# Kernel optimization log

Hardware: AMD Instinct MI355X
Metric: run time of the kernel (lower is better)

Reference implementation:

```python
import jax, jax.numpy as jnp
import numpy as np

B, S, D = 8, 4096, 1024
H = 16
HD = D // H          # 64
FF = 128             # FeedForward default intermediate_size
EPS = 1e-6           # flax RMSNorm default


def _rmsnorm(x, g):
    return x * jax.lax.rsqrt(jnp.mean(x * x, axis=-1, keepdims=True) + EPS) * g


def setup_inputs() -> dict:
    key = jax.random.key(0)
    ks = jax.random.split(key, 12)
    s = 0.02
    return {
        "x": jax.random.normal(ks[0], (B, S, D), jnp.float32),
        "attention_mask": jnp.ones((B, HD), jnp.int32),
        # per-head QKV projections stacked over heads: [H, D, HD]
        "Wq": jax.random.normal(ks[1], (H, D, HD), jnp.float32) * s,
        "bq": jnp.zeros((H, HD), jnp.float32),
        "Wk": jax.random.normal(ks[2], (H, D, HD), jnp.float32) * s,
        "bk": jnp.zeros((H, HD), jnp.float32),
        "Wv": jax.random.normal(ks[3], (H, D, HD), jnp.float32) * s,
        "bv": jnp.zeros((H, HD), jnp.float32),
        "Wo": jax.random.normal(ks[4], (D, D), jnp.float32) * s,
        "bo": jnp.zeros((D,), jnp.float32),
        "W1": jax.random.normal(ks[5], (D, FF), jnp.float32) * s,
        "b1": jnp.zeros((FF,), jnp.float32),
        "W2": jax.random.normal(ks[6], (FF, D), jnp.float32) * s,
        "b2": jnp.zeros((D,), jnp.float32),
        "g1": jnp.ones((D,), jnp.float32),
        "g2": jnp.ones((D,), jnp.float32),
    }


def reference(x, attention_mask, Wq, bq, Wk, bk, Wv, bv, Wo, bo, W1, b1, W2, b2, g1, g2):
    # per-head projections, vectorized over heads: [B, H, S, HD]
    q = jnp.einsum('bsd,hde->bhse', x, Wq) + bq[:, None, :]
    k = jnp.einsum('bsd,hde->bhse', x, Wk) + bk[:, None, :]
    v = jnp.einsum('bsd,hde->bhse', x, Wv) + bv[:, None, :]
    # scores = k^T @ q -> [B, H, HD(kfeat), HD(qfeat)]  (feature-feature attention)
    scores = jnp.einsum('bhsk,bhsq->bhkq', k, q)
    # tiled mask: each row of [HD, HD] equals mask -> masks along last (q-feature) axis
    m = attention_mask[:, None, None, :]  # [B,1,1,HD]
    scores = jnp.where(m == 0, -jnp.inf, scores)
    w = jax.nn.softmax(scores / jnp.sqrt(jnp.float32(HD)), axis=-2)
    # out = v @ w -> [B, H, S, HD]
    attn = jnp.einsum('bhsk,bhkq->bhsq', v, w)
    attn = attn.transpose(0, 2, 1, 3).reshape(B, S, D)  # concat heads
    # output projection + residual + RMSNorm
    h = x + attn @ Wo + bo
    h = _rmsnorm(h, g1)
    # tanh FFN + residual + RMSNorm
    ff = jnp.tanh(h @ W1 + b1) @ W2 + b2
    out = _rmsnorm(h + ff, g2)
    return out
```

## Files before the change

### kernel.cpp

```cpp
#include <hip/hip_runtime.h>
#include <math.h>

typedef __attribute__((ext_vector_type(4))) float f32x4;
typedef __attribute__((ext_vector_type(8))) short short8;
typedef __attribute__((ext_vector_type(4))) short short4v;

__device__ __forceinline__ float b2f(unsigned short u) {
  unsigned int x = ((unsigned int)u) << 16;
  return __builtin_bit_cast(float, x);
}
__device__ __forceinline__ unsigned short f2b(float f) {
  unsigned int x = __builtin_bit_cast(unsigned int, f);
  x += 0x7fffu + ((x >> 16) & 1u);
  return (unsigned short)(x >> 16);
}

__device__ __forceinline__ void gload16(const unsigned short* g, unsigned short* l) {
  __builtin_amdgcn_global_load_lds(
      (__attribute__((address_space(1))) void*)(unsigned long long)(const void*)g,
      (__attribute__((address_space(3))) void*)l, 16, 0, 0);
}

#define BARR  { __builtin_amdgcn_sched_barrier(0); __builtin_amdgcn_s_barrier(); __builtin_amdgcn_sched_barrier(0); }
#define LBARR { __builtin_amdgcn_sched_barrier(0); asm volatile("s_waitcnt lgkmcnt(0)" ::: "memory"); __builtin_amdgcn_s_barrier(); __builtin_amdgcn_sched_barrier(0); }
#define VMW(n) { __builtin_amdgcn_sched_barrier(0); asm volatile("s_waitcnt vmcnt(" #n ")" ::: "memory"); __builtin_amdgcn_sched_barrier(0); }

__global__ __launch_bounds__(256) void prep_kernel(
    const float* __restrict__ x, unsigned short* __restrict__ xb,
    const float* __restrict__ Wq, const float* __restrict__ Wk,
    const float* __restrict__ Wv, const float* __restrict__ Wo,
    const float* __restrict__ W1, const float* __restrict__ W2,
    const float* __restrict__ bq, const float* __restrict__ bk, const float* __restrict__ bv,
    const float* __restrict__ g1,
    unsigned short* __restrict__ BqkT, unsigned short* __restrict__ WoT,
    unsigned short* __restrict__ W1T, unsigned short* __restrict__ W2T,
    unsigned short* __restrict__ WvR,
    float* __restrict__ bqkv) {
  __shared__ float tile[64][65];
  int nb = blockIdx.x, t = threadIdx.x;
  if (nb < 16384) {
    long i = (long)nb * 256 + t;
    f32x4 a = ((const f32x4*)x)[i * 2];
    f32x4 b = ((const f32x4*)x)[i * 2 + 1];
    short8 o;
#pragma unroll
    for (int j = 0; j < 4; ++j) { o[j] = (short)f2b(a[j]); o[4 + j] = (short)f2b(b[j]); }
    ((short8*)xb)[i] = o;
    return;
  }
  int n0 = nb - 16384;
  if (n0 == 1088) {
#pragma unroll
    for (int it = 0; it < 12; ++it) {
      int idx = it * 256 + t;
      float v = (idx < 1024) ? bq[idx] : (idx < 2048 ? bk[idx - 1024] : bv[idx - 2048]);
      bqkv[idx] = v;
    }
    return;
  }
  if (n0 >= 832) {
    int rem = n0 - 832, h = rem >> 4, dc = rem & 15;
    int r = t >> 2, c0 = (t & 3) * 16;
    const float* s = Wv + ((long)h * 1024 + dc * 64 + r) * 64 + c0;
    unsigned short* d = WvR + (long)(dc * 64 + r) * 1024 + h * 64 + c0;
#pragma unroll
    for (int j4 = 0; j4 < 4; ++j4) {
      f32x4 v = *(const f32x4*)(s + j4 * 4);
      short4v o;
#pragma unroll
      for (int j = 0; j < 4; ++j) o[j] = (short)f2b(v[j]);
      *(short4v*)(d + j4 * 4) = o;
    }
    return;
  }
  const float* src; unsigned short* dst; int sld, dld;
  bool foldg = false; int dbase = 0;
  if (n0 < 512) {
    int w = n0 >> 8, rem = n0 & 255, h = rem >> 4, dc = rem & 15;
    const float* W = (w == 0) ? Wq : Wk;
    src = W + ((long)h * 1024 + dc * 64) * 64;                 sld = 64;
    dst = BqkT + (long)(w * 1024 + h * 64) * 1024 + dc * 64;   dld = 1024;
  } else if (n0 < 768) {
    int rem = n0 - 512, dr = rem >> 4, jc = rem & 15;
    src = Wo + (long)dr * 64 * 1024 + jc * 64;                 sld = 1024;
    dst = WoT + (long)jc * 64 * 1024 + dr * 64;                dld = 1024;
  } else if (n0 < 800) {
    int rem = n0 - 768, dr = rem >> 1, fc = rem & 1;
    src = W1 + (long)dr * 64 * 128 + fc * 64;                  sld = 128;
    dst = W1T + (long)fc * 64 * 1024 + dr * 64;                dld = 1024;
    foldg = true; dbase = dr * 64;
  } else {
    int rem = n0 - 800, fr = rem >> 4, jc = rem & 15;
    src = W2 + (long)fr * 64 * 1024 + jc * 64;                 sld = 1024;
    dst = W2T + (long)jc * 64 * 128 + fr * 64;                 dld = 128;
  }
  int r = t >> 2, c0 = (t & 3) * 16;
#pragma unroll
  for (int j4 = 0; j4 < 4; ++j4) {
    f32x4 v = *(const f32x4*)(src + (long)r * sld + c0 + j4 * 4);
    tile[c0 + j4 * 4 + 0][r] = v[0];
    tile[c0 + j4 * 4 + 1][r] = v[1];
    tile[c0 + j4 * 4 + 2][r] = v[2];
    tile[c0 + j4 * 4 + 3][r] = v[3];
  }
  __syncthreads();
  short8 o0, o1;
#pragma unroll
  for (int j = 0; j < 8; ++j) {
    float v0 = tile[r][c0 + j], v1 = tile[r][c0 + 8 + j];
    if (foldg) { v0 *= g1[dbase + c0 + j]; v1 *= g1[dbase + c0 + 8 + j]; }
    o0[j] = (short)f2b(v0);
    o1[j] = (short)f2b(v1);
  }
  *(short8*)(dst + (long)r * dld + c0) = o0;
  *(short8*)(dst + (long)r * dld + c0 + 8) = o1;
}

__device__ __forceinline__ void rdA2(short8 (&dst)[4][2], const char* paK0,
                                     const char* paK1, int off) {
#pragma unroll
  for (int fr = 0; fr < 4; ++fr) {
    dst[fr][0] = *(const short8*)(paK0 + off + fr * 2048);
    dst[fr][1] = *(const short8*)(paK1 + off + fr * 2048);
  }
}
__device__ __forceinline__ void rdB2(short8 (&dst)[2][2], const char* pbK0,
                                     const char* pbK1, int off) {
#pragma unroll
  for (int gr = 0; gr < 2; ++gr) {
    dst[gr][0] = *(const short8*)(pbK0 + off + gr * 2048);
    dst[gr][1] = *(const short8*)(pbK1 + off + gr * 2048);
  }
}
template <int BPH>
__device__ __forceinline__ void mfmaq_f(const short8 (&afr)[4][2], const short8 (&bf)[2][2],
                                        f32x4 (*ac)[4]) {
  __builtin_amdgcn_s_setprio(1);
#pragma unroll
  for (int fi = 0; fi < 4; ++fi)
#pragma unroll
    for (int gj = 0; gj < 2; ++gj)
#pragma unroll
      for (int ks = 0; ks < 2; ++ks)
        ac[fi][BPH * 2 + gj] = __builtin_amdgcn_mfma_f32_16x16x32_bf16(
            afr[fi][ks], bf[gj][ks], ac[fi][BPH * 2 + gj], 0, 0, 0);
  __builtin_amdgcn_s_setprio(0);
}

template <int EPI, int BSEL, int BBIAS>
__global__ __launch_bounds__(512, 2) void gemm8p(
    const unsigned short* __restrict__ A, int lda,
    const unsigned short* __restrict__ Bt, int ldb,
    unsigned short* __restrict__ C, int ldc,
    const float* __restrict__ bias,
    const unsigned short* __restrict__ residb, int ldr,
    const float* __restrict__ rs, const float* __restrict__ g1f,
    int K, int NBX) {
  extern __shared__ char smb[];
  const int tid = threadIdx.x;
  const int lane = tid & 63, wid = tid >> 6;
  const int wm = wid >> 2, wn = wid & 3;

  int orig = blockIdx.x;
  int xcd = orig & 7, j = orig >> 3;
  int perx = gridDim.x >> 3;
  int mpx = perx / NBX;
  int ms = j / (4 * NBX), nb = (j >> 2) % NBX, mq = j & 3;
  const long m0 = (long)(xcd * mpx + ms * 4 + mq) * 256;
  const long n0 = (long)nb * 256;
  const unsigned short* bt = BSEL ? (Bt + (m0 >> 12) * 1048576) : Bt;
  const float* biasp = BBIAS ? (bias + (m0 >> 12) * 1024) : bias;

  const int NT = K >> 6, NI = NT >> 1;

  const int lr = lane & 15, lc = (lane >> 4) * 16;
  const int eA = lc ^ ((lr & 7) << 4);
  const char* paK0 = smb + wm * 8192 + lr * 128 + eA;
  const char* paK1 = smb + wm * 8192 + lr * 128 + (eA ^ 64);
  const char* pbK0 = smb + 65536 + wn * 4096 + lr * 128 + eA;
  const char* pbK1 = smb + 65536 + wn * 4096 + lr * 128 + (eA ^ 64);

  short8 afr0[4][2], afr1[4][2];
  short8 bfr0[2][2], bfr1[2][2];
  f32x4 acc[8][4] = {};

  auto stA = [&](int buf, int ph, int kt) {
#pragma unroll
    for (int rnd = 0; rnd < 2; ++rnd) {
      int o = rnd * 8192 + tid * 16;
      int wms = o >> 13, rsw = (o >> 7) & 63, cb = o & 127;
      int pcb = cb ^ ((rsw & 7) << 4);
      const unsigned short* src = A + (m0 + wms * 128 + ph * 64 + rsw) * (long)lda + kt * 64 + (pcb >> 1);
      gload16(src, (unsigned short*)(smb + buf * 32768 + ph * 16384 + o));
    }
  };
  auto stB = [&](int buf, int ph, int kt) {
#pragma unroll
    for (int rnd = 0; rnd < 2; ++rnd) {
      int o = rnd * 8192 + tid * 16;
      int wns = (o >> 12) & 3, rsw = (o >> 7) & 31, cb = o & 127;
      int pcb = cb ^ ((rsw & 7) << 4);
      const unsigned short* src = bt + (n0 + wns * 64 + ph * 32 + rsw) * (long)ldb + kt * 64 + (pcb >> 1);
      gload16(src, (unsigned short*)(smb + 65536 + buf * 32768 + ph * 16384 + o));
    }
  };

  stA(0, 0, 0); stA(0, 1, 0); stB(0, 0, 0); stB(0, 1, 0);
  stA(1, 0, 1); stA(1, 1, 1); stB(1, 0, 1); stB(1, 1, 1);
  VMW(8);
  BARR;
  rdA2(afr0, paK0, paK1, 0);
  rdB2(bfr0, pbK0, pbK1, 0);

  for (int i = 0; i < NI; ++i) {
    int t2 = 2 * i + 2, t3 = 2 * i + 3;
    bool more = t2 < NT;
    LBARR;
    rdB2(bfr1, pbK0, pbK1, 16384);
    mfmaq_f<0>(afr0, bfr0, &acc[0]);
    LBARR;
    rdA2(afr1, paK0, paK1, 16384);
    mfmaq_f<1>(afr0, bfr1, &acc[0]);
    LBARR;
    if (more) { stA(0, 0, t2); stA(0, 1, t2); }
    mfmaq_f<0>(afr1, bfr0, &acc[4]);
    if (more) { VMW(4); } else { VMW(0); }
    LBARR;
    rdA2(afr0, paK0, paK1, 32768);
    rdB2(bfr0, pbK0, pbK1, 32768);
    if (more) { stB(0, 0, t2); stB(0, 1, t2); }
    mfmaq_f<1>(afr1, bfr1, &acc[4]);
    LBARR;
    rdB2(bfr1, pbK0, pbK1, 32768 + 16384);
    mfmaq_f<0>(afr0, bfr0, &acc[0]);
    LBARR;
    rdA2(afr1, paK0, paK1, 32768 + 16384);
    mfmaq_f<1>(afr0, bfr1, &acc[0]);
    LBARR;
    if (more) { stA(1, 0, t3); stA(1, 1, t3); }
    mfmaq_f<0>(afr1, bfr0, &acc[4]);
    if (more) { VMW(4); } else { VMW(0); }
    LBARR;
    if (more) { rdA2(afr0, paK0, paK1, 0); rdB2(bfr0, pbK0, pbK1, 0); }
    if (more) { stB(1, 0, t3); stB(1, 1, t3); }
    mfmaq_f<1>(afr1, bfr1, &acc[4]);
  }

#pragma unroll
  for (int f = 0; f < 8; ++f) {
#pragma unroll
    for (int g = 0; g < 4; ++g) {
      long col = n0 + wn * 64 + g * 16 + (lane & 15);
      float bv = (EPI == 6) ? 0.0f : biasp[col];
      float gv = (EPI == 5) ? g1f[col] : 0.0f;
#pragma unroll
      for (int r = 0; r < 4; ++r) {
        long row = m0 + wm * 128 + f * 16 + (lane >> 4) * 4 + r;
        float o = acc[f][g][r] + bv;
        if (EPI == 3) o += b2f(residb[row * (long)ldr + col]);
        if (EPI == 5) o += b2f(residb[row * (long)ldr + col]) * rs[row] * gv;
        C[row * (long)ldc + col] = f2b(o);
      }
    }
  }
}

template <int EPI>
__global__ __launch_bounds__(256, 2) void gemm_bt(
    const unsigned short* __restrict__ A, int lda,
    const unsigned short* __restrict__ Bt, int ldb,
    unsigned short* __restrict__ C, int ldc,
    const float* __restrict__ bias, const float* __restrict__ rs, int K) {
  __shared__ __align__(16) unsigned short Asm[128 * 32];
  __shared__ __align__(16) unsigned short Bsm[128 * 32];
  const int tid = threadIdx.x;
  const int lane = tid & 63, wid = tid >> 6;
  const int wr = wid >> 1, wc = wid & 1;
  const long m0 = (long)blockIdx.y * 128;
  const long n0 = (long)blockIdx.x * 128;

  f32x4 acc[4][4] = {};

  for (int kk = 0; kk < K; kk += 32) {
    __syncthreads();
#pragma unroll
    for (int i = 0; i < 2; ++i) {
      int slot = i * 256 + tid;
      int r = slot >> 2, cg = (slot & 3) * 8;
      gload16(A + (m0 + r) * (long)lda + kk + cg, &Asm[slot * 8]);
      gload16(Bt + (n0 + r) * (long)ldb + kk + cg, &Bsm[slot * 8]);
    }
    __syncthreads();
    short8 af[4], bfr[4];
#pragma unroll
    for (int mt = 0; mt < 4; ++mt)
      af[mt] = *(const short8*)&Asm[(wr * 64 + mt * 16 + (lane & 15)) * 32 + (lane >> 4) * 8];
#pragma unroll
    for (int nt = 0; nt < 4; ++nt)
      bfr[nt] = *(const short8*)&Bsm[(wc * 64 + nt * 16 + (lane & 15)) * 32 + (lane >> 4) * 8];
#pragma unroll
    for (int mt = 0; mt < 4; ++mt)
#pragma unroll
      for (int nt = 0; nt < 4; ++nt)
        acc[mt][nt] = __builtin_amdgcn_mfma_f32_16x16x32_bf16(af[mt], bfr[nt], acc[mt][nt], 0, 0, 0);
  }

  const long row0 = m0 + wr * 64 + ((lane >> 4) * 4);
  const long col0 = n0 + wc * 64 + (lane & 15);
#pragma unroll
  for (int mt = 0; mt < 4; ++mt) {
#pragma unroll
    for (int nt = 0; nt < 4; ++nt) {
      long col = col0 + nt * 16;
      float bv = bias[col];
      f32x4 v = acc[mt][nt];
#pragma unroll
      for (int r = 0; r < 4; ++r) {
        long row = row0 + mt * 16 + r;
        float o = v[r];
        if (EPI == 4) o = tanhf(o * rs[row] + bv);
        else o += bv;
        C[row * (long)ldc + col] = f2b(o);
      }
    }
  }
}

__device__ __forceinline__ int sperm(int e) { return ((e + (e >> 3)) & 7) << 4; }

__global__ __launch_bounds__(256) void scores_mfma(
    const unsigned short* __restrict__ QK, float* __restrict__ part) {
  __shared__ __align__(16) char lds[32768];
  int bh = blockIdx.x, seg = blockIdx.y;
  int b = bh >> 4, h = bh & 15;
  int tid = threadIdx.x, lane = tid & 63, wid = tid >> 6;
  int e0 = (tid & 7) * 8;
  int sl0 = (tid >> 3) * 4;
  const unsigned short* Qg = QK + h * 64;
  const unsigned short* Kg = QK + 1024 + h * 64;
  f32x4 acc[4] = {};

  for (int ch = 0; ch < 8; ++ch) {
    long S0 = (long)b * 4096 + seg * 1024 + ch * 128;
    __syncthreads();
    short8 kv0 = *(const short8*)(Kg + (S0 + sl0 + 0) * 2048 + e0);
    short8 kv1 = *(const short8*)(Kg + (S0 + sl0 + 1) * 2048 + e0);
    short8 kv2 = *(const short8*)(Kg + (S0 + sl0 + 2) * 2048 + e0);
    short8 kv3 = *(const short8*)(Kg + (S0 + sl0 + 3) * 2048 + e0);
    short8 qv0 = *(const short8*)(Qg + (S0 + sl0 + 0) * 2048 + e0);
    short8 qv1 = *(const short8*)(Qg + (S0 + sl0 + 1) * 2048 + e0);
    short8 qv2 = *(const short8*)(Qg + (S0 + sl0 + 2) * 2048 + e0);
    short8 qv3 = *(const short8*)(Qg + (S0 + sl0 + 3) * 2048 + e0);
#pragma unroll
    for (int je = 0; je < 8; ++je) {
      int e = e0 + je;
      int sw = sperm(e);
      char* rowK = lds + e * 256;
      char* rowQ = lds + 16384 + e * 256;
      unsigned int klo = (unsigned short)kv0[je] | ((unsigned int)(unsigned short)kv1[je] << 16);
      unsigned int khi = (unsigned short)kv2[je] | ((unsigned int)(unsigned short)kv3[je] << 16);
      unsigned int qlo = (unsigned short)qv0[je] | ((unsigned int)(unsigned short)qv1[je] << 16);
      unsigned int qhi = (unsigned short)qv2[je] | ((unsigned int)(unsigned short)qv3[je] << 16);
      *(unsigned int*)(rowK + ((sl0 * 2) ^ sw)) = klo;
      *(unsigned int*)(rowK + ((sl0 * 2 + 4) ^ sw)) = khi;
      *(unsigned int*)(rowQ + ((sl0 * 2) ^ sw)) = qlo;
      *(unsigned int*)(rowQ + ((sl0 * 2 + 4) ^ sw)) = qhi;
    }
    __syncthreads();
#pragma unroll
    for (int ksi = 0; ksi < 4; ++ksi) {
      int colb = ksi * 64 + (lane >> 4) * 16;
      int erA = wid * 16 + (lane & 15);
      short8 af = *(const short8*)(lds + erA * 256 + (colb ^ sperm(erA)));
#pragma unroll
      for (int n = 0; n < 4; ++n) {
        int erB = n * 16 + (lane & 15);
        short8 bf = *(const short8*)(lds + 16384 + erB * 256 + (colb ^ sperm(erB)));
        acc[n] = __builtin_amdgcn_mfma_f32_16x16x32_bf16(af, bf, acc[n], 0, 0, 0);
      }
    }
  }
  float* dst = part + ((long)bh * 4 + seg) * 4096;
#pragma unroll
  for (int n = 0; n < 4; ++n)
#pragma unroll
    for (int r = 0; r < 4; ++r) {
      int k = wid * 16 + (lane >> 4) * 4 + r;
      int q = n * 16 + (lane & 15);
      dst[k * 64 + q] = acc[n][r];
    }
}

__global__ __launch_bounds__(64) void softmax_Wb(
    const float* __restrict__ part, const int* __restrict__ mask,
    unsigned short* __restrict__ Wb) {
  __shared__ float lt[64][65];
  int bh = blockIdx.x, q = threadIdx.x;
  int b = bh >> 4;
  const float* p0 = part + (long)bh * 4 * 4096;
  float s[64];
#pragma unroll
  for (int k = 0; k < 64; ++k)
    s[k] = p0[k * 64 + q] + p0[4096 + k * 64 + q] + p0[8192 + k * 64 + q] + p0[12288 + k * 64 + q];
  bool live = (mask[b * 64 + q] != 0);
  float m = -1e30f;
#pragma unroll
  for (int k = 0; k < 64; ++k) m = fmaxf(m, s[k]);
  float sum = 0.0f;
#pragma unroll
  for (int k = 0; k < 64; ++k) {
    s[k] = __expf((s[k] - m) * 0.125f);
    sum += s[k];
  }
  float inv = live ? 1.0f / sum : 0.0f;
#pragma unroll
  for (int k = 0; k < 64; ++k) lt[k][q] = s[k] * inv;
  __syncthreads();
  unsigned short* o = Wb + (long)bh * 4096 + q * 64;
#pragma unroll
  for (int j8 = 0; j8 < 8; ++j8) {
    short8 ov;
#pragma unroll
    for (int j = 0; j < 8; ++j) ov[j] = (short)f2b(lt[q][j8 * 8 + j]);
    *(short8*)(o + j8 * 8) = ov;
  }
}

__global__ __launch_bounds__(256) void wpt_kernel(
    const unsigned short* __restrict__ WoT, const unsigned short* __restrict__ Wb,
    unsigned short* __restrict__ WPT) {
  int dblk = blockIdx.x;
  int h = blockIdx.y;
  int b = blockIdx.z;
  int tid = threadIdx.x, lane = tid & 63, wid = tid >> 6;
  int d0 = dblk * 256 + wid * 64;
  const unsigned short* wb = Wb + (long)(b * 16 + h) * 4096;
  f32x4 acc[4][4] = {};
#pragma unroll
  for (int ks = 0; ks < 2; ++ks) {
    short8 bf[4];
#pragma unroll
    for (int nt = 0; nt < 4; ++nt)
      bf[nt] = *(const short8*)(wb + (nt * 16 + (lane & 15)) * 64 + ks * 32 + (lane >> 4) * 8);
#pragma unroll
    for (int mt = 0; mt < 4; ++mt) {
      short8 af = *(const short8*)(WoT + (long)(d0 + mt * 16 + (lane & 15)) * 1024 + h * 64 + ks * 32 + (lane >> 4) * 8);
#pragma unroll
      for (int nt = 0; nt < 4; ++nt)
        acc[mt][nt] = __builtin_amdgcn_mfma_f32_16x16x32_bf16(af, bf[nt], acc[mt][nt], 0, 0, 0);
    }
  }
#pragma unroll
  for (int mt = 0; mt < 4; ++mt)
#pragma unroll
    for (int nt = 0; nt < 4; ++nt)
#pragma unroll
      for (int r = 0; r < 4; ++r) {
        long row = d0 + mt * 16 + (lane >> 4) * 4 + r;
        int col = h * 64 + nt * 16 + (lane & 15);
        WPT[(long)b * 1048576 + row * 1024 + col] = f2b(acc[mt][nt][r]);
      }
}

__global__ __launch_bounds__(256) void bvdot_kernel(
    const unsigned short* __restrict__ WPT, const float* __restrict__ bv,
    const float* __restrict__ bo, float* __restrict__ hb) {
  int b = blockIdx.y;
  int dp = blockIdx.x * 256 + threadIdx.x;
  const unsigned short* row = WPT + (long)b * 1048576 + (long)dp * 1024;
  float acc = 0.0f;
#pragma unroll 4
  for (int c = 0; c < 1024; c += 8) {
    short8 v = *(const short8*)(row + c);
#pragma unroll
    for (int j = 0; j < 8; ++j) acc += b2f((unsigned short)v[j]) * bv[c + j];
  }
  hb[b * 1024 + dp] = bo[dp] + acc;
}

__global__ __launch_bounds__(256) void rowscale_k(
    const unsigned short* __restrict__ in, float* __restrict__ rs) {
  long row = blockIdx.x;
  int tid = threadIdx.x;
  short4v u = *(const short4v*)(in + row * 1024 + tid * 4);
  float ss = 0.0f;
#pragma unroll
  for (int i = 0; i < 4; ++i) {
    float v = b2f((unsigned short)u[i]);
    ss += v * v;
  }
#pragma unroll
  for (int off = 32; off > 0; off >>= 1) ss += __shfl_xor(ss, off, 64);
  __shared__ float wsum[4];
  if ((tid & 63) == 0) wsum[tid >> 6] = ss;
  __syncthreads();
  if (tid == 0) {
    float tot = wsum[0] + wsum[1] + wsum[2] + wsum[3];
    rs[row] = rsqrtf(tot * (1.0f / 1024.0f) + 1e-6f);
  }
}

__global__ __launch_bounds__(256) void rmsnorm_k(
    const unsigned short* __restrict__ in, const float* __restrict__ g,
    float* __restrict__ outf) {
  long row = blockIdx.x;
  int tid = threadIdx.x;
  short4v u = *(const short4v*)(in + row * 1024 + tid * 4);
  float v[4];
  float ss = 0.0f;
#pragma unroll
  for (int i = 0; i < 4; ++i) {
    v[i] = b2f((unsigned short)u[i]);
    ss += v[i] * v[i];
  }
#pragma unroll
  for (int off = 32; off > 0; off >>= 1) ss += __shfl_xor(ss, off, 64);
  __shared__ float wsum[4];
  if ((tid & 63) == 0) wsum[tid >> 6] = ss;
  __syncthreads();
  float tot = wsum[0] + wsum[1] + wsum[2] + wsum[3];
  float rsv = rsqrtf(tot * (1.0f / 1024.0f) + 1e-6f);
  f32x4 gv = *(const f32x4*)(g + tid * 4);
  f32x4 ov;
#pragma unroll
  for (int i = 0; i < 4; ++i) ov[i] = v[i] * rsv * gv[i];
  *(f32x4*)(outf + row * 1024 + tid * 4) = ov;
}

extern "C" void kernel_launch(void* const* d_in, const int* in_sizes, int n_in,
                              void* d_out, int out_size, void* d_ws, size_t ws_size,
                              hipStream_t stream) {
  const float* x  = (const float*)d_in[0];
  const int* mask = (const int*)d_in[1];
  const float* Wq = (const float*)d_in[2];
  const float* bq = (const float*)d_in[3];
  const float* Wk = (const float*)d_in[4];
  const float* bk = (const float*)d_in[5];
  const float* Wv = (const float*)d_in[6];
  const float* bv = (const float*)d_in[7];
  const float* Wo = (const float*)d_in[8];
  const float* bo = (const float*)d_in[9];
  const float* W1 = (const float*)d_in[10];
  const float* b1 = (const float*)d_in[11];
  const float* W2 = (const float*)d_in[12];
  const float* b2 = (const float*)d_in[13];
  const float* g1 = (const float*)d_in[14];
  const float* g2 = (const float*)d_in[15];

  char* ws = (char*)d_ws;
  size_t off = 0;
  auto alc = [&](size_t n) { size_t o = off; off += (n + 255) & ~(size_t)255; return o; };
  unsigned short* BqkT  = (unsigned short*)(ws + alc(2048UL * 1024 * 2));
  unsigned short* WoT   = (unsigned short*)(ws + alc(1024UL * 1024 * 2));
  unsigned short* W1T   = (unsigned short*)(ws + alc(128UL * 1024 * 2));
  unsigned short* W2T   = (unsigned short*)(ws + alc(1024UL * 128 * 2));
  unsigned short* WvR   = (unsigned short*)(ws + alc(1024UL * 1024 * 2));
  float*          bqkv  = (float*)(ws + alc(3072UL * 4));
  float*          HBb   = (float*)(ws + alc(8192UL * 4));
  unsigned short* R0    = (unsigned short*)(ws + alc(32768UL * 1024 * 2));
  unsigned short* R1    = (unsigned short*)(ws + alc(32768UL * 2048 * 2));
  unsigned short* R2    = (unsigned short*)(ws + alc(32768UL * 1024 * 2));
  unsigned short* WPb   = (unsigned short*)(ws + alc(8UL * 1048576 * 2));
  unsigned short* WVPb  = (unsigned short*)(ws + alc(8UL * 1048576 * 2));
  unsigned short* Tb    = (unsigned short*)(ws + alc(32768UL * 128 * 2));
  float*          SP    = (float*)(ws + alc(512UL * 4096 * 4));
  unsigned short* Wbuf  = (unsigned short*)(ws + alc(128UL * 4096 * 2));
  float*          RSb   = (float*)(ws + alc(32768UL * 4));
  if (ws_size < off) return;

  unsigned short* xb   = R0;
  unsigned short* HFb  = R0;
  unsigned short* QKb  = R1;
  unsigned short* H1b  = R2;
  float* outp = (float*)d_out;

  prep_kernel<<<17473, 256, 0, stream>>>(x, xb, Wq, Wk, Wv, Wo, W1, W2, bq, bk, bv, g1,
                                         BqkT, WoT, W1T, W2T, WvR, bqkv);
  gemm8p<0, 0, 0><<<1024, 512, 131072, stream>>>(xb, 1024, BqkT, 1024, QKb, 2048,
                                                 bqkv, nullptr, 0, nullptr, nullptr,
                                                 1024, 8);
  scores_mfma<<<dim3(128, 4), 256, 0, stream>>>(QKb, SP);
  softmax_Wb<<<128, 64, 0, stream>>>(SP, mask, Wbuf);
  wpt_kernel<<<dim3(4, 16, 8), 256, 0, stream>>>(WoT, Wbuf, WPb);
  gemm8p<6, 0, 0><<<128, 512, 131072, stream>>>(WPb, 1024, WvR, 1024, WVPb, 1024,
                                                nullptr, nullptr, 0, nullptr, nullptr,
                                                1024, 4);
  bvdot_kernel<<<dim3(4, 8), 256, 0, stream>>>(WPb, bqkv + 2048, bo, HBb);
  gemm8p<3, 1, 1><<<512, 512, 131072, stream>>>(xb, 1024, WVPb, 1024, H1b, 1024,
                                                HBb, xb, 1024, nullptr, nullptr,
                                                1024, 4);
  rowscale_k<<<32768, 256, 0, stream>>>(H1b, RSb);
  gemm_bt<4><<<dim3(1, 256), 256, 0, stream>>>(H1b, 1024, W1T, 1024, Tb, 128, b1, RSb, 1024);
  gemm8p<5, 0, 0><<<512, 512, 131072, stream>>>(Tb, 128, W2T, 128, HFb, 1024,
                                                b2, H1b, 1024, RSb, g1,
                                                128, 4);
  rmsnorm_k<<<32768, 256, 0, stream>>>(HFb, g2, outp);
}
```

Measured before the change: 466.5 us.

## Fuse row sum-of-squares and bias dot into GEMM epilogues via atomics

Result: faster. 453.7 us (median of 2 runs) (-2.7%).

```diff
diff --git a/kernel.cpp b/kernel.cpp
--- a/kernel.cpp
+++ b/kernel.cpp
@@ -154,7 +154,7 @@
     unsigned short* __restrict__ C, int ldc,
     const float* __restrict__ bias,
     const unsigned short* __restrict__ residb, int ldr,
-    const float* __restrict__ rs, const float* __restrict__ g1f,
+    float* __restrict__ ssb, const float* __restrict__ aux,
     int K, int NBX) {
   extern __shared__ char smb[];
   const int tid = threadIdx.x;
@@ -248,18 +248,38 @@
 
 #pragma unroll
   for (int f = 0; f < 8; ++f) {
+    float ssp[4] = {0.0f, 0.0f, 0.0f, 0.0f};
 #pragma unroll
     for (int g = 0; g < 4; ++g) {
       long col = n0 + wn * 64 + g * 16 + (lane & 15);
       float bv = (EPI == 6) ? 0.0f : biasp[col];
-      float gv = (EPI == 5) ? g1f[col] : 0.0f;
+      if (EPI == 7) bv += aux[col];
+      float gv = (EPI == 5) ? aux[col] : 0.0f;
 #pragma unroll
       for (int r = 0; r < 4; ++r) {
         long row = m0 + wm * 128 + f * 16 + (lane >> 4) * 4 + r;
         float o = acc[f][g][r] + bv;
-        if (EPI == 3) o += b2f(residb[row * (long)ldr + col]);
-        if (EPI == 5) o += b2f(residb[row * (long)ldr + col]) * rs[row] * gv;
+        if (EPI == 7) o += b2f(residb[row * (long)ldr + col]);
+        if (EPI == 5) {
+          float rsv = rsqrtf(ssb[row] * (1.0f / 1024.0f) + 1e-6f);
+          o += b2f(residb[row * (long)ldr + col]) * rsv * gv;
+        }
+        if (EPI == 7) ssp[r] += o * o;
         C[row * (long)ldc + col] = f2b(o);
+      }
+    }
+    if (EPI == 7) {
+#pragma unroll
+      for (int r = 0; r < 4; ++r) {
+        float p = ssp[r];
+        p += __shfl_xor(p, 1, 64);
+        p += __shfl_xor(p, 2, 64);
+        p += __shfl_xor(p, 4, 64);
+        p += __shfl_xor(p, 8, 64);
+        if ((lane & 15) == 0) {
+          long row = m0 + wm * 128 + f * 16 + (lane >> 4) * 4 + r;
+          atomicAdd(&ssb[row], p);
+        }
       }
     }
   }
@@ -270,7 +290,7 @@
     const unsigned short* __restrict__ A, int lda,
     const unsigned short* __restrict__ Bt, int ldb,
     unsigned short* __restrict__ C, int ldc,
-    const float* __restrict__ bias, const float* __restrict__ rs, int K) {
+    const float* __restrict__ bias, const float* __restrict__ ssb, int K) {
   __shared__ __align__(16) unsigned short Asm[128 * 32];
   __shared__ __align__(16) unsigned short Bsm[128 * 32];
   const int tid = threadIdx.x;
@@ -318,8 +338,10 @@
       for (int r = 0; r < 4; ++r) {
         long row = row0 + mt * 16 + r;
         float o = v[r];
-        if (EPI == 4) o = tanhf(o * rs[row] + bv);
-        else o += bv;
+        if (EPI == 4) {
+          float rsv = rsqrtf(ssb[row] * (1.0f / 1024.0f) + 1e-6f);
+          o = tanhf(o * rsv + bv);
+        } else o += bv;
         C[row * (long)ldc + col] = f2b(o);
       }
     }
@@ -428,7 +450,8 @@
 
 __global__ __launch_bounds__(256) void wpt_kernel(
     const unsigned short* __restrict__ WoT, const unsigned short* __restrict__ Wb,
-    unsigned short* __restrict__ WPT) {
+    unsigned short* __restrict__ WPT, const float* __restrict__ bv,
+    float* __restrict__ hb) {
   int dblk = blockIdx.x;
   int h = blockIdx.y;
   int b = blockIdx.z;
@@ -450,53 +473,27 @@
         acc[mt][nt] = __builtin_amdgcn_mfma_f32_16x16x32_bf16(af, bf[nt], acc[mt][nt], 0, 0, 0);
     }
   }
-#pragma unroll
-  for (int mt = 0; mt < 4; ++mt)
-#pragma unroll
-    for (int nt = 0; nt < 4; ++nt)
-#pragma unroll
-      for (int r = 0; r < 4; ++r) {
-        long row = d0 + mt * 16 + (lane >> 4) * 4 + r;
-        int col = h * 64 + nt * 16 + (lane & 15);
-        WPT[(long)b * 1048576 + row * 1024 + col] = f2b(acc[mt][nt][r]);
+  float bvv[4];
+#pragma unroll
+  for (int nt = 0; nt < 4; ++nt) bvv[nt] = bv[h * 64 + nt * 16 + (lane & 15)];
+#pragma unroll
+  for (int mt = 0; mt < 4; ++mt) {
+#pragma unroll
+    for (int r = 0; r < 4; ++r) {
+      long row = d0 + mt * 16 + (lane >> 4) * 4 + r;
+      float p = 0.0f;
+#pragma unroll
+      for (int nt = 0; nt < 4; ++nt) {
+        float o = acc[mt][nt][r];
+        WPT[(long)b * 1048576 + row * 1024 + h * 64 + nt * 16 + (lane & 15)] = f2b(o);
+        p += o * bvv[nt];
       }
-}
-
-__global__ __launch_bounds__(256) void bvdot_kernel(
-    const unsigned short* __restrict__ WPT, const float* __restrict__ bv,
-    const float* __restrict__ bo, float* __restrict__ hb) {
-  int b = blockIdx.y;
-  int dp = blockIdx.x * 256 + threadIdx.x;
-  const unsigned short* row = WPT + (long)b * 1048576 + (long)dp * 1024;
-  float acc = 0.0f;
-#pragma unroll 4
-  for (int c = 0; c < 1024; c += 8) {
-    short8 v = *(const short8*)(row + c);
-#pragma unroll
-    for (int j = 0; j < 8; ++j) acc += b2f((unsigned short)v[j]) * bv[c + j];
-  }
-  hb[b * 1024 + dp] = bo[dp] + acc;
-}
-
-__global__ __launch_bounds__(256) void rowscale_k(
-    const unsigned short* __restrict__ in, float* __restrict__ rs) {
-  long row = blockIdx.x;
-  int tid = threadIdx.x;
-  short4v u = *(const short4v*)(in + row * 1024 + tid * 4);
-  float ss = 0.0f;
-#pragma unroll
-  for (int i = 0; i < 4; ++i) {
-    float v = b2f((unsigned short)u[i]);
-    ss += v * v;
-  }
-#pragma unroll
-  for (int off = 32; off > 0; off >>= 1) ss += __shfl_xor(ss, off, 64);
-  __shared__ float wsum[4];
-  if ((tid & 63) == 0) wsum[tid >> 6] = ss;
-  __syncthreads();
-  if (tid == 0) {
-    float tot = wsum[0] + wsum[1] + wsum[2] + wsum[3];
-    rs[row] = rsqrtf(tot * (1.0f / 1024.0f) + 1e-6f);
+      p += __shfl_xor(p, 1, 64);
+      p += __shfl_xor(p, 2, 64);
+      p += __shfl_xor(p, 4, 64);
+      p += __shfl_xor(p, 8, 64);
+      if ((lane & 15) == 0) atomicAdd(&hb[b * 1024 + row], p);
+    }
   }
 }
 
@@ -565,7 +562,7 @@
   unsigned short* Tb    = (unsigned short*)(ws + alc(32768UL * 128 * 2));
   float*          SP    = (float*)(ws + alc(512UL * 4096 * 4));
   unsigned short* Wbuf  = (unsigned short*)(ws + alc(128UL * 4096 * 2));
-  float*          RSb   = (float*)(ws + alc(32768UL * 4));
+  float*          SSb   = (float*)(ws + alc(32768UL * 4));
   if (ws_size < off) return;
 
   unsigned short* xb   = R0;
@@ -574,6 +571,8 @@
   unsigned short* H1b  = R2;
   float* outp = (float*)d_out;
 
+  hipMemsetAsync(HBb, 0, 8192 * 4, stream);
+  hipMemsetAsync(SSb, 0, 32768 * 4, stream);
   prep_kernel<<<17473, 256, 0, stream>>>(x, xb, Wq, Wk, Wv, Wo, W1, W2, bq, bk, bv, g1,
                                          BqkT, WoT, W1T, W2T, WvR, bqkv);
   gemm8p<0, 0, 0><<<1024, 512, 131072, stream>>>(xb, 1024, BqkT, 1024, QKb, 2048,
@@ -581,18 +580,16 @@
                                                  1024, 8);
   scores_mfma<<<dim3(128, 4), 256, 0, stream>>>(QKb, SP);
   softmax_Wb<<<128, 64, 0, stream>>>(SP, mask, Wbuf);
-  wpt_kernel<<<dim3(4, 16, 8), 256, 0, stream>>>(WoT, Wbuf, WPb);
+  wpt_kernel<<<dim3(4, 16, 8), 256, 0, stream>>>(WoT, Wbuf, WPb, bqkv + 2048, HBb);
   gemm8p<6, 0, 0><<<128, 512, 131072, stream>>>(WPb, 1024, WvR, 1024, WVPb, 1024,
                                                 nullptr, nullptr, 0, nullptr, nullptr,
                                                 1024, 4);
-  bvdot_kernel<<<dim3(4, 8), 256, 0, stream>>>(WPb, bqkv + 2048, bo, HBb);
-  gemm8p<3, 1, 1><<<512, 512, 131072, stream>>>(xb, 1024, WVPb, 1024, H1b, 1024,
-                                                HBb, xb, 1024, nullptr, nullptr,
+  gemm8p<7, 1, 1><<<512, 512, 131072, stream>>>(xb, 1024, WVPb, 1024, H1b, 1024,
+                                                HBb, xb, 1024, SSb, bo,
                                                 1024, 4);
-  rowscale_k<<<32768, 256, 0, stream>>>(H1b, RSb);
-  gemm_bt<4><<<dim3(1, 256), 256, 0, stream>>>(H1b, 1024, W1T, 1024, Tb, 128, b1, RSb, 1024);
+  gemm_bt<4><<<dim3(1, 256), 256, 0, stream>>>(H1b, 1024, W1T, 1024, Tb, 128, b1, SSb, 1024);
   gemm8p<5, 0, 0><<<512, 512, 131072, stream>>>(Tb, 128, W2T, 128, HFb, 1024,
-                                                b2, H1b, 1024, RSb, g1,
+                                                b2, H1b, 1024, SSb, g1,
                                                 128, 4);
   rmsnorm_k<<<32768, 256, 0, stream>>>(HFb, g2, outp);
 }
```
